# Kernel optimization log

Hardware: AMD Instinct MI355X
Metric: run time of the kernel (lower is better)

Reference implementation:

```python
import jax, jax.numpy as jnp
import numpy as np

HIDDEN = 4096
N_HEADS = 32
N_KV_HEADS = 8
HEAD_DIM = HIDDEN // N_HEADS  # 128
ROPE_THETA = 10000.0
BATCH, SEQ = 2, 2048


def setup_inputs() -> dict:
    key = jax.random.key(0)
    ks = jax.random.split(key, 5)
    s = 0.02
    return {
        "hidden_states": jax.random.normal(ks[0], (BATCH, SEQ, HIDDEN), jnp.float32),
        "position_ids": jnp.broadcast_to(jnp.arange(SEQ, dtype=jnp.int32), (BATCH, SEQ)),
        "Wq": jax.random.normal(ks[1], (HIDDEN, HIDDEN), jnp.float32) * s,
        "Wk": jax.random.normal(ks[2], (N_KV_HEADS * HEAD_DIM, HIDDEN), jnp.float32) * s,
        "Wv": jax.random.normal(ks[3], (N_KV_HEADS * HEAD_DIM, HIDDEN), jnp.float32) * s,
        "Wo": jax.random.normal(ks[4], (HIDDEN, HIDDEN), jnp.float32) * s,
    }


def _rope_cos_sin(position_ids, dtype):
    # HF LlamaRotaryEmbedding: inv_freq over even dims, emb = concat(freqs, freqs)
    inv_freq = 1.0 / (ROPE_THETA ** (jnp.arange(0, HEAD_DIM, 2, dtype=jnp.float32) / HEAD_DIM))
    freqs = position_ids.astype(jnp.float32)[..., None] * inv_freq[None, None, :]  # [B,S,D/2]
    emb = jnp.concatenate([freqs, freqs], axis=-1)  # [B,S,D]
    return jnp.cos(emb).astype(dtype), jnp.sin(emb).astype(dtype)


def _rotate_half(x):
    x1, x2 = jnp.split(x, 2, axis=-1)
    return jnp.concatenate([-x2, x1], axis=-1)


def reference(hidden_states, position_ids, Wq, Wk, Wv, Wo):
    B, S, _ = hidden_states.shape
    dtype = hidden_states.dtype

    # QKV projections (nn.Linear: x @ W.T), reshape to [B, H, S, D]
    q = (hidden_states @ Wq.T).reshape(B, S, N_HEADS, HEAD_DIM).transpose(0, 2, 1, 3)
    k = (hidden_states @ Wk.T).reshape(B, S, N_KV_HEADS, HEAD_DIM).transpose(0, 2, 1, 3)
    v = (hidden_states @ Wv.T).reshape(B, S, N_KV_HEADS, HEAD_DIM).transpose(0, 2, 1, 3)

    # RoPE
    cos, sin = _rope_cos_sin(position_ids, dtype)  # [B,S,D]
    cos_b, sin_b = cos[:, None, :, :], sin[:, None, :, :]
    q = q * cos_b + _rotate_half(q) * sin_b
    k = k * cos_b + _rotate_half(k) * sin_b

    # GQA: group queries over shared kv heads instead of materializing repeat_kv
    groups = N_HEADS // N_KV_HEADS
    qg = q.reshape(B, N_KV_HEADS, groups, S, HEAD_DIM)

    scale = 1.0 / jnp.sqrt(jnp.asarray(HEAD_DIM, dtype=jnp.float32)).astype(dtype)
    scores = jnp.einsum('bkgqd,bkld->bkgql', qg, k) * scale  # [B,KV,G,S,S]

    causal = jnp.tril(jnp.ones((S, S), dtype=bool))
    scores = jnp.where(causal[None, None, None], scores, jnp.asarray(-jnp.inf, scores.dtype))
    probs = jax.nn.softmax(scores.astype(jnp.float32), axis=-1).astype(dtype)

    out = jnp.einsum('bkgql,bkld->bkgqd', probs, v)  # [B,KV,G,S,D]
    out = out.reshape(B, N_HEADS, S, HEAD_DIM).transpose(0, 2, 1, 3).reshape(B, S, HIDDEN)
    return out @ Wo.T
```

## Files before the change

### kernel.cpp

```cpp
#include <hip/hip_runtime.h>
#include <cstdint>
#include <cstddef>

typedef unsigned short u16;
typedef short bf16x8 __attribute__((ext_vector_type(8)));
typedef float f32x4 __attribute__((ext_vector_type(4)));

#define HIDDEN 4096
#define NH 32
#define NKV 8
#define HD 128
#define SEQL 2048
#define BATCH 2
#define NTOK (BATCH*SEQL)
#define QKVN (HIDDEN + 2*NKV*HD)

#define QKS 136

__device__ __forceinline__ u16 f2bf(float f){
    unsigned u = __float_as_uint(f);
    u += 0x7FFF + ((u >> 16) & 1);
    return (u16)(u >> 16);
}
__device__ __forceinline__ float bf2f(u16 h){
    return __uint_as_float(((unsigned)h) << 16);
}
__device__ __forceinline__ f32x4 zero4(){
    f32x4 z; z[0]=0.f; z[1]=0.f; z[2]=0.f; z[3]=0.f; return z;
}

typedef const unsigned int __attribute__((address_space(1)))* gas1_t;
typedef unsigned int __attribute__((address_space(3)))* las3_t;
__device__ __forceinline__ void gload_lds16(const u16* g, u16* l){
    __builtin_amdgcn_global_load_lds((gas1_t)g, (las3_t)l, 16, 0, 0);
}

__global__ __launch_bounds__(256) void cvt_kernel(const float* __restrict__ src,
                                                  u16* __restrict__ dst, int n4){
    int i = blockIdx.x * 256 + threadIdx.x;
    if (i < n4){
        float4 v = ((const float4*)src)[i];
        ushort4 o;
        o.x = f2bf(v.x); o.y = f2bf(v.y); o.z = f2bf(v.z); o.w = f2bf(v.w);
        ((ushort4*)dst)[i] = o;
    }
}

template<int OUT_BF16>
__global__ __launch_bounds__(512) void gemm8_bt(const u16* __restrict__ A,
                                                const u16* __restrict__ B,
                                                void* __restrict__ Cp,
                                                int M, int N, int K){
    __shared__ __align__(16) u16 L[2][2][256*64];
    int tid = threadIdx.x;
    int wave = tid >> 6, lane = tid & 63, quad = lane >> 4, l16 = lane & 15;
    int wm = wave >> 2, wn = wave & 3;

    int nwg = gridDim.x;
    int cpx = nwg >> 3;
    int orig = blockIdx.x;
    int wg = (orig & 7) * cpx + (orig >> 3);
    int nbx = N >> 8;
    int bx = wg % nbx, by = wg / nbx;
    size_t row0 = (size_t)by * 256, col0 = (size_t)bx * 256;

    int r0 = tid >> 3, cc = (tid & 7) ^ (r0 & 7);
    const u16* aS0 = A + (row0 + r0) * (size_t)K + cc * 8;
    const u16* bS0 = B + (col0 + r0) * (size_t)K + cc * 8;
    u16* ldsd = &L[0][0][0] + tid * 8;

#define STAGE_HALF(mat, half, bufi, kt) do {                                        \
        const u16* g_ = ((mat) ? bS0 : aS0) + (size_t)((half)*128) * K + (size_t)(kt) * 64; \
        u16* d_ = ldsd + (bufi)*32768 + (mat)*16384 + (half)*8192;                  \
        gload_lds16(g_, d_);                                                        \
        gload_lds16(g_ + (size_t)64 * K, d_ + 4096);                                \
    } while(0)

    const int nt = K >> 6;

    int swz0 = ((0*4 + quad) ^ (l16 & 7)) * 8;
    int swz1 = ((1*4 + quad) ^ (l16 & 7)) * 8;

    f32x4 acc[8][4];
    #pragma unroll
    for (int i=0;i<8;i++)
        #pragma unroll
        for (int j=0;j<4;j++) acc[i][j] = zero4();

    STAGE_HALF(1,0,0,0); STAGE_HALF(1,1,0,0);
    STAGE_HALF(0,0,0,0); STAGE_HALF(0,1,0,0);
    STAGE_HALF(1,0,1,1); STAGE_HALF(1,1,1,1);

    bf16x8 bF[4][2];
    for (int t = 0; t < nt; ++t){
        if (t < nt - 1) asm volatile("s_waitcnt vmcnt(4)" ::: "memory");
        else            asm volatile("s_waitcnt vmcnt(0)" ::: "memory");
        __builtin_amdgcn_s_barrier();
        const u16* bufA = &L[t & 1][0][0];
        const u16* bufB = &L[t & 1][1][0];

        #pragma unroll
        for (int p = 0; p < 4; ++p){
            bf16x8 aF[2][2];
            if (p == 0){
                #pragma unroll
                for (int ni = 0; ni < 4; ++ni){
                    int rb = (wn*64 + ni*16 + l16) * 64;
                    bF[ni][0] = *(const bf16x8*)(bufB + rb + swz0);
                    bF[ni][1] = *(const bf16x8*)(bufB + rb + swz1);
                }
            }
            #pragma unroll
            for (int i = 0; i < 2; ++i){
                int ra = (wm*128 + p*32 + i*16 + l16) * 64;
                aF[i][0] = *(const bf16x8*)(bufA + ra + swz0);
                aF[i][1] = *(const bf16x8*)(bufA + ra + swz1);
            }
            if (p == 0){ if (t + 1 < nt) STAGE_HALF(0, 0, (t+1)&1, t+1); }
            if (p == 1){ if (t + 1 < nt) STAGE_HALF(0, 1, (t+1)&1, t+1); }
            if (p == 2){ if (t + 2 < nt) STAGE_HALF(1, 0, t&1, t+2); }
            if (p == 3){ if (t + 2 < nt) STAGE_HALF(1, 1, t&1, t+2); }

            __builtin_amdgcn_sched_barrier(0);
            __builtin_amdgcn_s_barrier();
            __builtin_amdgcn_sched_barrier(0);
            __builtin_amdgcn_s_setprio(1);
            #pragma unroll
            for (int ni = 0; ni < 4; ++ni)
                #pragma unroll
                for (int i = 0; i < 2; ++i){
                    acc[p*2+i][ni] = __builtin_amdgcn_mfma_f32_16x16x32_bf16(aF[i][0], bF[ni][0], acc[p*2+i][ni], 0, 0, 0);
                    acc[p*2+i][ni] = __builtin_amdgcn_mfma_f32_16x16x32_bf16(aF[i][1], bF[ni][1], acc[p*2+i][ni], 0, 0, 0);
                }
            __builtin_amdgcn_s_setprio(0);
            __builtin_amdgcn_sched_barrier(0);
            asm volatile("s_waitcnt lgkmcnt(0)" ::: "memory");
            if (p < 3) __builtin_amdgcn_s_barrier();
        }
    }
#undef STAGE_HALF

    #pragma unroll
    for (int mi = 0; mi < 8; ++mi)
        #pragma unroll
        for (int ni = 0; ni < 4; ++ni){
            size_t row = row0 + wm*128 + mi*16 + quad*4;
            size_t col = col0 + wn*64 + ni*16 + l16;
            #pragma unroll
            for (int r = 0; r < 4; ++r){
                if (OUT_BF16) ((u16*)Cp)[(row + r) * (size_t)N + col] = f2bf(acc[mi][ni][r]);
                else          ((float*)Cp)[(row + r) * (size_t)N + col] = acc[mi][ni][r];
            }
        }
}

__global__ __launch_bounds__(256) void rope_kernel(u16* __restrict__ qkv,
                                                   const int* __restrict__ pos_ids){
    int idx = blockIdx.x * 256 + threadIdx.x;
    if (idx < 8388608){
        int tok = idx >> 11;
        int rem = idx & 2047;
        int h = rem >> 6, d = rem & 63;
        size_t base = (size_t)tok * QKVN + h * 128 + d;
        float v1 = bf2f(qkv[base]), v2 = bf2f(qkv[base + 64]);
        float p = (float)pos_ids[tok];
        float invf = exp2f((float)d * -0.2076205059304601f);
        float fr = p * invf;
        float s, c; __sincosf(fr, &s, &c);
        qkv[base]      = f2bf(v1 * c - v2 * s);
        qkv[base + 64] = f2bf(v2 * c + v1 * s);
    } else {
        int i2 = idx - 8388608;
        int tok = i2 >> 9;
        int rem = i2 & 511;
        int kv = rem >> 6, d = rem & 63;
        size_t base = (size_t)tok * QKVN + HIDDEN + kv * 128 + d;
        float v1 = bf2f(qkv[base]), v2 = bf2f(qkv[base + 64]);
        float p = (float)pos_ids[tok];
        float invf = exp2f((float)d * -0.2076205059304601f);
        float fr = p * invf;
        float s, c; __sincosf(fr, &s, &c);
        qkv[base]      = f2bf(v1 * c - v2 * s);
        qkv[base + 64] = f2bf(v2 * c + v1 * s);
    }
}

__global__ __launch_bounds__(256) void vtrans_kernel(const u16* __restrict__ qkv,
                                                     u16* __restrict__ Vt){
    int blk = blockIdx.x;
    int tt = blk & 31, bkv = blk >> 5;
    int b = bkv >> 3, kv = bkv & 7;
    const u16* src = qkv + (size_t)(b * SEQL + tt * 64) * QKVN + 5120 + kv * HD;
    u16* dst = Vt + ((size_t)(b * NKV + kv)) * HD * SEQL + tt * 64;
    int tid = threadIdx.x;
    for (int i = tid; i < 1024; i += 256){
        int d = i >> 3, sc = i & 7;
        u16 tmp[8];
        #pragma unroll
        for (int j = 0; j < 8; j++) tmp[j] = src[(size_t)(sc * 8 + j) * QKVN + d];
        *(uint4*)(dst + (size_t)d * SEQL + sc * 8) = *(const uint4*)tmp;
    }
}

__global__ __launch_bounds__(256) void attn_kernel(const u16* __restrict__ qkv,
                                                   const u16* __restrict__ Vt,
                                                   u16* __restrict__ outb){
    __shared__ __align__(16) u16 Ks[64*128];
    __shared__ __align__(16) u16 Vs[128*64];
    __shared__ __align__(16) u16 Ps[4][16*QKS];

    int qt = 31 - (blockIdx.x >> 6);
    int bh = blockIdx.x & 63;
    int h  = bh & 31;
    int b  = bh >> 5;
    int kvh = h >> 2;
    int tid = threadIdx.x, wave = tid >> 6, lane = tid & 63;
    int quad = lane >> 4, l16 = lane & 15;
    int q0 = qt * 64, qrow = q0 + wave * 16;

    const u16* Qg  = qkv + (size_t)(b * SEQL + qrow + l16) * QKVN + h * HD;
    const u16* Kg0 = qkv + (size_t)(b * SEQL) * QKVN + HIDDEN + kvh * HD;
    const u16* Vg  = Vt + ((size_t)(b * NKV + kvh)) * HD * SEQL;
    u16* Pw = &Ps[wave][0];

    const float scale = 0.08838834764831845f;
    bf16x8 qf[4];
    #pragma unroll
    for (int c = 0; c < 4; c++){
        bf16x8 q = *(const bf16x8*)(Qg + c * 32 + quad * 8);
        #pragma unroll
        for (int e = 0; e < 8; e++){
            float f = bf2f((u16)q[e]) * scale;
            q[e] = (short)f2bf(f);
        }
        qf[c] = q;
    }

    const u16* kg[4]; u16* kd[4];
    const u16* vg[4]; u16* vd[4];
    {
        int r4 = lane >> 4, s16 = lane & 15;
        int r8 = lane >> 3, s8 = lane & 7;
        #pragma unroll
        for (int i = 0; i < 4; i++){
            int lr = wave * 16 + i * 4 + r4;
            int cK = s16 ^ (lr & 15);
            kg[i] = Kg0 + (size_t)lr * QKVN + cK * 8;
            kd[i] = Ks + lr * 128 + s16 * 8;
            int dr = wave * 32 + i * 8 + r8;
            int cV = s8 ^ (dr & 7);
            vg[i] = Vg + (size_t)dr * SEQL + cV * 8;
            vd[i] = Vs + dr * 64 + s8 * 8;
        }
    }

    float m_i[4] = {-INFINITY, -INFINITY, -INFINITY, -INFINITY};
    float l_i[4] = {0.f, 0.f, 0.f, 0.f};
    f32x4 Oacc[8];
    #pragma unroll
    for (int t=0;t<8;t++) Oacc[t] = zero4();

    int kend = q0 + 64;
    size_t kOffK = 0;
    for (int k0 = 0; k0 < kend; k0 += 64, kOffK += (size_t)64 * QKVN){
        __syncthreads();
        #pragma unroll
        for (int i = 0; i < 4; i++) gload_lds16(kg[i] + kOffK, kd[i]);
        #pragma unroll
        for (int i = 0; i < 4; i++) gload_lds16(vg[i] + k0, vd[i]);
        __syncthreads();

        f32x4 st[4];
        #pragma unroll
        for (int t=0;t<4;t++) st[t] = zero4();
        #pragma unroll
        for (int c4 = 0; c4 < 4; c4++){
            int cw = c4 * 4 + quad;
            #pragma unroll
            for (int t = 0; t < 4; t++){
                bf16x8 bk = *(const bf16x8*)(Ks + (t*16 + l16)*128 + (cw ^ l16)*8);
                st[t] = __builtin_amdgcn_mfma_f32_16x16x32_bf16(qf[c4], bk, st[t], 0, 0, 0);
            }
        }

        bool needmask = (k0 + 63 >= qrow);
        int row_g = qrow + quad * 4;
        float alpha[4];
        #pragma unroll
        for (int r=0;r<4;r++){
            float mx = m_i[r];
            #pragma unroll
            for (int t=0;t<4;t++){
                float v = st[t][r];
                if (needmask){
                    int col = k0 + t*16 + l16;
                    v = (col <= row_g + r) ? v : -INFINITY;
                }
                st[t][r] = v;
                mx = fmaxf(mx, v);
            }
            #pragma unroll
            for (int m=8;m>=1;m>>=1) mx = fmaxf(mx, __shfl_xor(mx, m));
            float mnew = mx;
            alpha[r] = __expf(m_i[r] - mnew);
            float rs = 0.f;
            #pragma unroll
            for (int t=0;t<4;t++){
                float pv = __expf(st[t][r] - mnew);
                st[t][r] = pv;
                rs += pv;
            }
            #pragma unroll
            for (int m=8;m>=1;m>>=1) rs += __shfl_xor(rs, m);
            l_i[r] = l_i[r] * alpha[r] + rs;
            m_i[r] = mnew;
        }

        #pragma unroll
        for (int t=0;t<8;t++)
            #pragma unroll
            for (int r=0;r<4;r++) Oacc[t][r] *= alpha[r];

        #pragma unroll
        for (int t=0;t<4;t++)
            #pragma unroll
            for (int r=0;r<4;r++)
                Pw[(quad*4 + r)*QKS + t*16 + l16] = f2bf(st[t][r]);

        #pragma unroll
        for (int c2 = 0; c2 < 2; c2++){
            bf16x8 ap = *(const bf16x8*)(Pw + l16*QKS + c2*32 + quad*8);
            int cw = c2 * 4 + quad;
            #pragma unroll
            for (int t = 0; t < 8; t++){
                int d = t*16 + l16;
                bf16x8 bv = *(const bf16x8*)(Vs + d*64 + (cw ^ (l16 & 7))*8);
                Oacc[t] = __builtin_amdgcn_mfma_f32_16x16x32_bf16(ap, bv, Oacc[t], 0, 0, 0);
            }
        }
    }

    float invl[4];
    #pragma unroll
    for (int r=0;r<4;r++) invl[r] = 1.f / l_i[r];
    int row0 = qrow + quad * 4;
    #pragma unroll
    for (int t=0;t<8;t++)
        #pragma unroll
        for (int r=0;r<4;r++){
            size_t o = ((size_t)(b * SEQL + row0 + r)) * HIDDEN + h * HD + t*16 + l16;
            outb[o] = f2bf(Oacc[t][r] * invl[r]);
        }
}

extern "C" void kernel_launch(void* const* d_in, const int* in_sizes, int n_in,
                              void* d_out, int out_size, void* d_ws, size_t ws_size,
                              hipStream_t stream){
    (void)in_sizes; (void)n_in; (void)out_size; (void)ws_size;
    const float* hs  = (const float*)d_in[0];
    const int*   pos = (const int*)d_in[1];
    const float* Wq  = (const float*)d_in[2];
    const float* Wk  = (const float*)d_in[3];
    const float* Wv  = (const float*)d_in[4];
    const float* Wo  = (const float*)d_in[5];
    float* out = (float*)d_out;
    char* ws = (char*)d_ws;

    u16* Xbf  = (u16*)(ws);
    u16* Wqkv = (u16*)(ws + 33554432);
    u16* Wob  = (u16*)(ws + 83886080);
    u16* QKVb = (u16*)(ws + 117440512);
    u16* Vt   = (u16*)(ws + 167772160);
    u16* attn_bf = Xbf;

    cvt_kernel<<<16384, 256, 0, stream>>>(hs, Xbf, 4194304);
    cvt_kernel<<<16384, 256, 0, stream>>>(Wq, Wqkv, 4194304);
    cvt_kernel<<<4096,  256, 0, stream>>>(Wk, Wqkv + (size_t)4096*4096, 1048576);
    cvt_kernel<<<4096,  256, 0, stream>>>(Wv, Wqkv + (size_t)5120*4096, 1048576);
    cvt_kernel<<<16384, 256, 0, stream>>>(Wo, Wob, 4194304);

    gemm8_bt<1><<<384, 512, 0, stream>>>(Xbf, Wqkv, QKVb, NTOK, QKVN, HIDDEN);
    rope_kernel<<<40960, 256, 0, stream>>>(QKVb, pos);
    vtrans_kernel<<<512, 256, 0, stream>>>(QKVb, Vt);
    attn_kernel<<<BATCH*NH*(SEQL/64), 256, 0, stream>>>(QKVb, Vt, attn_bf);
    gemm8_bt<0><<<256, 512, 0, stream>>>(attn_bf, Wob, out, NTOK, HIDDEN, HIDDEN);
}
```

Baseline: 803.8 us.

## Double-buffer K/V tiles in attention with prefetch and MFMA priority hints

The attention kernel now keeps two LDS buffers for the K and V tiles. It issues the async global-to-LDS loads for the next tile before computing on the current one, and the first tile is loaded before Q is read. That leaves one barrier per iteration instead of two and is meant to hide global-load latency behind the QK and PV MFMAs. s_setprio raises wave priority around the MFMA loops. The P staging row stride shrinks from 136 to 68 elements, which cuts LDS use but leaves the 16-byte P row reads unaligned. Total LDS per block roughly doubles, which may lower the number of resident blocks.

```diff
diff --git a/kernel.cpp b/kernel.cpp
--- a/kernel.cpp
+++ b/kernel.cpp
@@ -15,7 +15,7 @@
 #define NTOK (BATCH*SEQL)
 #define QKVN (HIDDEN + 2*NKV*HD)
 
-#define QKS 136
+#define QKS 68
 
 __device__ __forceinline__ u16 f2bf(float f){
     unsigned u = __float_as_uint(f);
@@ -205,8 +205,8 @@
 __global__ __launch_bounds__(256) void attn_kernel(const u16* __restrict__ qkv,
                                                    const u16* __restrict__ Vt,
                                                    u16* __restrict__ outb){
-    __shared__ __align__(16) u16 Ks[64*128];
-    __shared__ __align__(16) u16 Vs[128*64];
+    __shared__ __align__(16) u16 Ks[2][64*128];
+    __shared__ __align__(16) u16 Vs[2][128*64];
     __shared__ __align__(16) u16 Ps[4][16*QKS];
 
     int qt = 31 - (blockIdx.x >> 6);
@@ -223,19 +223,6 @@
     const u16* Vg  = Vt + ((size_t)(b * NKV + kvh)) * HD * SEQL;
     u16* Pw = &Ps[wave][0];
 
-    const float scale = 0.08838834764831845f;
-    bf16x8 qf[4];
-    #pragma unroll
-    for (int c = 0; c < 4; c++){
-        bf16x8 q = *(const bf16x8*)(Qg + c * 32 + quad * 8);
-        #pragma unroll
-        for (int e = 0; e < 8; e++){
-            float f = bf2f((u16)q[e]) * scale;
-            q[e] = (short)f2bf(f);
-        }
-        qf[c] = q;
-    }
-
     const u16* kg[4]; u16* kd[4];
     const u16* vg[4]; u16* vd[4];
     {
@@ -246,12 +233,30 @@
             int lr = wave * 16 + i * 4 + r4;
             int cK = s16 ^ (lr & 15);
             kg[i] = Kg0 + (size_t)lr * QKVN + cK * 8;
-            kd[i] = Ks + lr * 128 + s16 * 8;
+            kd[i] = &Ks[0][0] + lr * 128 + s16 * 8;
             int dr = wave * 32 + i * 8 + r8;
             int cV = s8 ^ (dr & 7);
             vg[i] = Vg + (size_t)dr * SEQL + cV * 8;
-            vd[i] = Vs + dr * 64 + s8 * 8;
-        }
+            vd[i] = &Vs[0][0] + dr * 64 + s8 * 8;
+        }
+    }
+
+    #pragma unroll
+    for (int i = 0; i < 4; i++) gload_lds16(kg[i], kd[i]);
+    #pragma unroll
+    for (int i = 0; i < 4; i++) gload_lds16(vg[i], vd[i]);
+
+    const float scale = 0.08838834764831845f;
+    bf16x8 qf[4];
+    #pragma unroll
+    for (int c = 0; c < 4; c++){
+        bf16x8 q = *(const bf16x8*)(Qg + c * 32 + quad * 8);
+        #pragma unroll
+        for (int e = 0; e < 8; e++){
+            float f = bf2f((u16)q[e]) * scale;
+            q[e] = (short)f2bf(f);
+        }
+        qf[c] = q;
     }
 
     float m_i[4] = {-INFINITY, -INFINITY, -INFINITY, -INFINITY};
@@ -260,28 +265,37 @@
     #pragma unroll
     for (int t=0;t<8;t++) Oacc[t] = zero4();
 
-    int kend = q0 + 64;
-    size_t kOffK = 0;
-    for (int k0 = 0; k0 < kend; k0 += 64, kOffK += (size_t)64 * QKVN){
+    const int nt = qt + 1;
+    for (int t = 0; t < nt; ++t){
+        int cur = t & 1;
         __syncthreads();
-        #pragma unroll
-        for (int i = 0; i < 4; i++) gload_lds16(kg[i] + kOffK, kd[i]);
-        #pragma unroll
-        for (int i = 0; i < 4; i++) gload_lds16(vg[i] + k0, vd[i]);
-        __syncthreads();
+        if (t + 1 < nt){
+            int nxt = (t + 1) & 1;
+            size_t kOff = (size_t)(t + 1) * 64 * QKVN;
+            int vOff = (t + 1) * 64;
+            #pragma unroll
+            for (int i = 0; i < 4; i++) gload_lds16(kg[i] + kOff, kd[i] + nxt * 8192);
+            #pragma unroll
+            for (int i = 0; i < 4; i++) gload_lds16(vg[i] + vOff, vd[i] + nxt * 8192);
+        }
+        const u16* Kc = &Ks[cur][0];
+        const u16* Vc = &Vs[cur][0];
+        int k0 = t * 64;
 
         f32x4 st[4];
         #pragma unroll
-        for (int t=0;t<4;t++) st[t] = zero4();
+        for (int s=0;s<4;s++) st[s] = zero4();
+        __builtin_amdgcn_s_setprio(1);
         #pragma unroll
         for (int c4 = 0; c4 < 4; c4++){
             int cw = c4 * 4 + quad;
             #pragma unroll
-            for (int t = 0; t < 4; t++){
-                bf16x8 bk = *(const bf16x8*)(Ks + (t*16 + l16)*128 + (cw ^ l16)*8);
-                st[t] = __builtin_amdgcn_mfma_f32_16x16x32_bf16(qf[c4], bk, st[t], 0, 0, 0);
-            }
-        }
+            for (int s = 0; s < 4; s++){
+                bf16x8 bk = *(const bf16x8*)(Kc + (s*16 + l16)*128 + (cw ^ l16)*8);
+                st[s] = __builtin_amdgcn_mfma_f32_16x16x32_bf16(qf[c4], bk, st[s], 0, 0, 0);
+            }
+        }
+        __builtin_amdgcn_s_setprio(0);
 
         bool needmask = (k0 + 63 >= qrow);
         int row_g = qrow + quad * 4;
@@ -290,13 +304,13 @@
         for (int r=0;r<4;r++){
             float mx = m_i[r];
             #pragma unroll
-            for (int t=0;t<4;t++){
-                float v = st[t][r];
+            for (int s=0;s<4;s++){
+                float v = st[s][r];
                 if (needmask){
-                    int col = k0 + t*16 + l16;
+                    int col = k0 + s*16 + l16;
                     v = (col <= row_g + r) ? v : -INFINITY;
                 }
-                st[t][r] = v;
+                st[s][r] = v;
                 mx = fmaxf(mx, v);
             }
             #pragma unroll
@@ -305,9 +319,9 @@
             alpha[r] = __expf(m_i[r] - mnew);
             float rs = 0.f;
             #pragma unroll
-            for (int t=0;t<4;t++){
-                float pv = __expf(st[t][r] - mnew);
-                st[t][r] = pv;
+            for (int s=0;s<4;s++){
+                float pv = __expf(st[s][r] - mnew);
+                st[s][r] = pv;
                 rs += pv;
             }
             #pragma unroll
@@ -317,27 +331,29 @@
         }
 
         #pragma unroll
-        for (int t=0;t<8;t++)
-            #pragma unroll
-            for (int r=0;r<4;r++) Oacc[t][r] *= alpha[r];
-
-        #pragma unroll
-        for (int t=0;t<4;t++)
+        for (int s=0;s<8;s++)
+            #pragma unroll
+            for (int r=0;r<4;r++) Oacc[s][r] *= alpha[r];
+
+        #pragma unroll
+        for (int s=0;s<4;s++)
             #pragma unroll
             for (int r=0;r<4;r++)
-                Pw[(quad*4 + r)*QKS + t*16 + l16] = f2bf(st[t][r]);
-
+                Pw[(quad*4 + r)*QKS + s*16 + l16] = f2bf(st[s][r]);
+
+        __builtin_amdgcn_s_setprio(1);
         #pragma unroll
         for (int c2 = 0; c2 < 2; c2++){
             bf16x8 ap = *(const bf16x8*)(Pw + l16*QKS + c2*32 + quad*8);
             int cw = c2 * 4 + quad;
             #pragma unroll
-            for (int t = 0; t < 8; t++){
-                int d = t*16 + l16;
-                bf16x8 bv = *(const bf16x8*)(Vs + d*64 + (cw ^ (l16 & 7))*8);
-                Oacc[t] = __builtin_amdgcn_mfma_f32_16x16x32_bf16(ap, bv, Oacc[t], 0, 0, 0);
-            }
-        }
+            for (int s = 0; s < 8; s++){
+                int d = s*16 + l16;
+                bf16x8 bv = *(const bf16x8*)(Vc + d*64 + (cw ^ (l16 & 7))*8);
+                Oacc[s] = __builtin_amdgcn_mfma_f32_16x16x32_bf16(ap, bv, Oacc[s], 0, 0, 0);
+            }
+        }
+        __builtin_amdgcn_s_setprio(0);
     }
 
     float invl[4];
@@ -345,11 +361,11 @@
     for (int r=0;r<4;r++) invl[r] = 1.f / l_i[r];
     int row0 = qrow + quad * 4;
     #pragma unroll
-    for (int t=0;t<8;t++)
+    for (int s=0;s<8;s++)
         #pragma unroll
         for (int r=0;r<4;r++){
-            size_t o = ((size_t)(b * SEQL + row0 + r)) * HIDDEN + h * HD + t*16 + l16;
-            outb[o] = f2bf(Oacc[t][r] * invl[r]);
+            size_t o = ((size_t)(b * SEQL + row0 + r)) * HIDDEN + h * HD + s*16 + l16;
+            outb[o] = f2bf(Oacc[s][r] * invl[r]);
         }
 }
 
```

Result: faster. 786.5 us (-2.2%).
